# Kernel optimization log

Hardware: AMD Instinct MI355X
Metric: run time of the kernel (lower is better)

The kernel has to match this reference:

```python
import jax, jax.numpy as jnp
import numpy as np

THRESH = 0.5
MARGIN = 0.1
SCALE_POS = 2.0
SCALE_NEG = 40.0
SCALE_POS_W = 1.0
SCALE_NEG_W = 1.0

B, D = 4096, 256
N_CLASSES = 64


def setup_inputs() -> dict:
    key = jax.random.key(0)
    k1, k2, k3 = jax.random.split(key, 3)
    feats = jax.random.normal(k1, (B, D), dtype=jnp.float32)
    sim_weight = jax.random.uniform(k2, (B, B), dtype=jnp.float32)
    labels = jax.random.randint(k3, (B,), 0, N_CLASSES, dtype=jnp.int64)
    return {"feats": feats, "sim_weight": sim_weight, "labels": labels}


def reference(feats, sim_weight, labels):
    # L2-normalize rows, cosine-similarity matrix [B, B]
    feats_norm = feats / jnp.linalg.norm(feats, axis=1, keepdims=True)
    sim = feats_norm @ feats_norm.T

    # pos mask includes the diagonal (labels[i] == labels[i]), matching torch code
    pos_mask = labels[:, None] == labels[None, :]
    neg_mask = ~pos_mask

    # per-row min positive similarity (pos set is never empty due to diagonal)
    min_pos = jnp.min(jnp.where(pos_mask, sim, jnp.inf), axis=1, keepdims=True)
    # per-row max negative similarity; only valid when row has a negative
    has_neg = jnp.any(neg_mask, axis=1, keepdims=True)
    max_neg = jnp.max(jnp.where(neg_mask, sim, -jnp.inf), axis=1, keepdims=True)

    # hard mining: keep negs harder than the easiest pos, pos harder than hardest neg
    neg_keep = neg_mask & (sim + MARGIN > min_pos)
    pos_keep = pos_mask & jnp.where(has_neg, sim - MARGIN < max_neg, True)

    # masked log-sum-exp style reductions (non-vanila path uses sim_weight)
    pos_exp = jnp.exp(-SCALE_POS * (sim - THRESH) + SCALE_POS_W * sim_weight)
    neg_exp = jnp.exp(SCALE_NEG * (sim - THRESH) - SCALE_NEG_W * sim_weight)
    pos_sum = jnp.sum(jnp.where(pos_keep, pos_exp, 0.0), axis=1)
    neg_sum = jnp.sum(jnp.where(neg_keep, neg_exp, 0.0), axis=1)

    pos_loss = jnp.log1p(pos_sum) / SCALE_POS
    neg_loss = jnp.log1p(neg_sum) / SCALE_NEG
    # rows with both sets empty contribute log1p(0)=0, matching the `continue`
    return jnp.sum(pos_loss + neg_loss) / feats.shape[0]
```

## Files before the change

### kernel.cpp

```cpp
#include <hip/hip_runtime.h>
#include <hip/hip_bf16.h>
#include <math.h>

#define B_SZ 4096
#define D_SZ 256
#define MARGIN   0.1f

typedef __attribute__((ext_vector_type(8))) __bf16 bf16x8;
typedef __attribute__((ext_vector_type(4))) float f32x4;
typedef __attribute__((ext_vector_type(8))) unsigned short u16x8;

__device__ __forceinline__ unsigned short f2bf(float f) {
    unsigned u = __float_as_uint(f);
    unsigned r = (u + 0x7FFFu + ((u >> 16) & 1u)) >> 16;
    return (unsigned short)r;
}

__device__ __forceinline__ void gload_lds16(const void* g, void* lds) {
    __builtin_amdgcn_global_load_lds(
        (const __attribute__((address_space(1))) void*)g,
        (__attribute__((address_space(3))) void*)lds, 16, 0, 0);
}

__global__ void norm_init_kernel(const float* __restrict__ feats,
                                 unsigned short* __restrict__ fb) {
    int row = blockIdx.x;
    int lane = threadIdx.x;
    const float4 v = *(const float4*)(feats + (size_t)row * D_SZ + lane * 4);
    float s = v.x * v.x + v.y * v.y + v.z * v.z + v.w * v.w;
#pragma unroll
    for (int m = 32; m; m >>= 1) s += __shfl_xor(s, m);
    float rinv = 1.0f / sqrtf(s);
    short4 st;
    st.x = (short)f2bf(v.x * rinv);
    st.y = (short)f2bf(v.y * rinv);
    st.z = (short)f2bf(v.z * rinv);
    st.w = (short)f2bf(v.w * rinv);
    *(short4*)(fb + (size_t)row * D_SZ + lane * 4) = st;
}

__device__ __forceinline__ void gemm_tile(const unsigned short* __restrict__ fb,
                                          unsigned short* lA0, unsigned short* lB0,
                                          int i0, int j0, int t, f32x4 acc[4][4]) {
    const int lane = t & 63, w = t >> 6;
    const int wr = w >> 1, wc = w & 1;
    const int fr = lane & 15, kg = lane >> 4;
    const int srow = lane >> 2, schunk = lane & 3;

#pragma unroll
    for (int m = 0; m < 4; ++m)
#pragma unroll
        for (int n = 0; n < 4; ++n) acc[m][n] = (f32x4){0.f, 0.f, 0.f, 0.f};

    auto stage = [&](int buf, int kc) {
#pragma unroll
        for (int half = 0; half < 2; ++half) {
            const int R0 = w * 32 + half * 16;
            const int row = R0 + srow;
            const int off = ((schunk ^ ((row >> 1) & 3)) << 3);
            gload_lds16(fb + (size_t)(i0 + row) * D_SZ + kc + off,
                        lA0 + buf * (128 * 32) + R0 * 32);
            gload_lds16(fb + (size_t)(j0 + row) * D_SZ + kc + off,
                        lB0 + buf * (128 * 32) + R0 * 32);
        }
    };

    stage(0, 0);
    asm volatile("s_waitcnt vmcnt(0)" ::: "memory");
    __syncthreads();

#pragma unroll
    for (int s = 0; s < 8; ++s) {
        const int cur = s & 1;
        if (s < 7) stage(cur ^ 1, (s + 1) * 32);
        const unsigned short* A  = lA0 + cur * (128 * 32);
        const unsigned short* Bp = lB0 + cur * (128 * 32);
        bf16x8 a[4], b[4];
#pragma unroll
        for (int m = 0; m < 4; ++m) {
            const int row = wr * 64 + m * 16 + fr;
            a[m] = *(const bf16x8*)(A + row * 32 + ((kg ^ ((row >> 1) & 3)) << 3));
        }
#pragma unroll
        for (int n = 0; n < 4; ++n) {
            const int row = wc * 64 + n * 16 + fr;
            b[n] = *(const bf16x8*)(Bp + row * 32 + ((kg ^ ((row >> 1) & 3)) << 3));
        }
#pragma unroll
        for (int m = 0; m < 4; ++m)
#pragma unroll
            for (int n = 0; n < 4; ++n)
                acc[m][n] = __builtin_amdgcn_mfma_f32_16x16x32_bf16(a[m], b[n], acc[m][n], 0, 0, 0);
        if (s < 7) {
            asm volatile("s_waitcnt vmcnt(0)" ::: "memory");
            __syncthreads();
        }
    }
}

__global__ __launch_bounds__(256, 4) void gemm_store_sym(const unsigned short* __restrict__ fb,
                                                         unsigned short* __restrict__ simb) {
    __shared__ unsigned short sm[2 * 128 * 32 * 2];
    const int t = threadIdx.x;

    int z = blockIdx.x, bi = 0;
    while (z >= 32 - bi) { z -= 32 - bi; ++bi; }
    const int bj = bi + z;
    const int i0 = bi * 128, j0 = bj * 128;

    f32x4 acc[4][4];
    gemm_tile(fb, sm, sm + 128 * 32 * 2, i0, j0, t, acc);

    const int lane = t & 63, w = t >> 6;
    const int wr = w >> 1, wc = w & 1, fr = lane & 15, kg = lane >> 4;

#pragma unroll
    for (int m = 0; m < 4; ++m)
#pragma unroll
        for (int r = 0; r < 4; ++r) {
            const size_t row = i0 + wr * 64 + m * 16 + kg * 4 + r;
#pragma unroll
            for (int n = 0; n < 4; ++n)
                simb[row * B_SZ + j0 + wc * 64 + n * 16 + fr] = f2bf(acc[m][n][r]);
        }

    if (bi == bj) return;

    __syncthreads();
    unsigned short* T = sm;
#pragma unroll
    for (int m = 0; m < 4; ++m) {
        const int rowbase = wr * 64 + m * 16 + kg * 4;
#pragma unroll
        for (int n = 0; n < 4; ++n) {
            const int col = wc * 64 + n * 16 + fr;
            short4 h;
            h.x = (short)f2bf(acc[m][n][0]);
            h.y = (short)f2bf(acc[m][n][1]);
            h.z = (short)f2bf(acc[m][n][2]);
            h.w = (short)f2bf(acc[m][n][3]);
            *(short4*)(T + col * 128 + (rowbase ^ ((col & 15) << 3))) = h;
        }
    }
    __syncthreads();

    const int r0 = t & 15, cb = t >> 4;
#pragma unroll
    for (int p = 0; p < 8; ++p) {
        const int c = cb + p * 16;
        u16x8 v = *(const u16x8*)(T + c * 128 + 8 * (r0 ^ (c & 15)));
        *(u16x8*)(simb + (size_t)(j0 + c) * B_SZ + i0 + r0 * 8) = v;
    }
}

__global__ __launch_bounds__(256) void row_pass(const unsigned short* __restrict__ simb,
                                                const float* __restrict__ simw,
                                                const int* __restrict__ labels,
                                                float* __restrict__ rowloss) {
    const int i = blockIdx.x, t = threadIdx.x;
    const int lane = t & 63, w = t >> 6;
    const int il = labels[i];
    float sv[16], wv[16];
    int lj[16];
    {
        const u16x8* sp = (const u16x8*)(simb + (size_t)i * B_SZ + t * 16);
        u16x8 s0 = sp[0], s1 = sp[1];
#pragma unroll
        for (int e = 0; e < 8; ++e) {
            sv[e]     = __uint_as_float((unsigned)s0[e] << 16);
            sv[8 + e] = __uint_as_float((unsigned)s1[e] << 16);
        }
        const float4* wp = (const float4*)(simw + (size_t)i * B_SZ + t * 16);
#pragma unroll
        for (int q = 0; q < 4; ++q) {
            float4 wq = wp[q];
            wv[q * 4 + 0] = wq.x; wv[q * 4 + 1] = wq.y;
            wv[q * 4 + 2] = wq.z; wv[q * 4 + 3] = wq.w;
        }
        const int4* lp = (const int4*)(labels + t * 16);
#pragma unroll
        for (int q = 0; q < 4; ++q) {
            int4 lq = lp[q];
            lj[q * 4 + 0] = lq.x; lj[q * 4 + 1] = lq.y;
            lj[q * 4 + 2] = lq.z; lj[q * 4 + 3] = lq.w;
        }
    }
    float mn = INFINITY, mx = -INFINITY;
#pragma unroll
    for (int e = 0; e < 16; ++e) {
        if (lj[e] == il) mn = fminf(mn, sv[e]);
        else             mx = fmaxf(mx, sv[e]);
    }
#pragma unroll
    for (int msk = 1; msk < 64; msk <<= 1) {
        mn = fminf(mn, __shfl_xor(mn, msk));
        mx = fmaxf(mx, __shfl_xor(mx, msk));
    }
    __shared__ float smn[4], smx[4], sps[4], sns[4];
    if (lane == 0) { smn[w] = mn; smx[w] = mx; }
    __syncthreads();
    mn = fminf(fminf(smn[0], smn[1]), fminf(smn[2], smn[3]));
    mx = fmaxf(fmaxf(smx[0], smx[1]), fmaxf(smx[2], smx[3]));
    const bool hasneg = (mx != -INFINITY);
    float ps = 0.f, ns = 0.f;
#pragma unroll
    for (int e = 0; e < 16; ++e) {
        const float s = sv[e];
        if (lj[e] == il) {
            if (!hasneg || (s - MARGIN < mx))
                ps += __expf(fmaf(-2.f, s, 1.f) + wv[e]);
        } else {
            if (s + MARGIN > mn)
                ns += __expf(fmaf(40.f, s, -20.f) - wv[e]);
        }
    }
#pragma unroll
    for (int msk = 1; msk < 64; msk <<= 1) {
        ps += __shfl_xor(ps, msk);
        ns += __shfl_xor(ns, msk);
    }
    if (lane == 0) { sps[w] = ps; sns[w] = ns; }
    __syncthreads();
    if (t == 0) {
        ps = sps[0] + sps[1] + sps[2] + sps[3];
        ns = sns[0] + sns[1] + sns[2] + sns[3];
        rowloss[i] = log1pf(ps) * 0.5f + log1pf(ns) * 0.025f;
    }
}

__global__ void final_big(const float* __restrict__ rowloss, float* __restrict__ out) {
    __shared__ float red[256];
    int t = threadIdx.x;
    float acc = 0.f;
    for (int i = t; i < B_SZ; i += 256) acc += rowloss[i];
    red[t] = acc;
    __syncthreads();
    for (int s = 128; s > 0; s >>= 1) {
        if (t < s) red[t] += red[t + s];
        __syncthreads();
    }
    if (t == 0) out[0] = red[0] / (float)B_SZ;
}

extern "C" void kernel_launch(void* const* d_in, const int* in_sizes, int n_in,
                              void* d_out, int out_size, void* d_ws, size_t ws_size,
                              hipStream_t stream) {
    const float* feats  = (const float*)d_in[0];
    const float* simw   = (const float*)d_in[1];
    const int*   labels = (const int*)d_in[2];
    float* out = (float*)d_out;

    char* ws = (char*)d_ws;
    float*    rowloss = (float*)ws;
    unsigned short* fb   = (unsigned short*)(ws + B_SZ * 4);
    unsigned short* simb = (unsigned short*)(ws + B_SZ * 4 + (size_t)B_SZ * D_SZ * 2);

    norm_init_kernel<<<B_SZ, 64, 0, stream>>>(feats, fb);

    gemm_store_sym<<<528, 256, 0, stream>>>(fb, simb);
    row_pass<<<B_SZ, 256, 0, stream>>>(simb, simw, labels, rowloss);
    final_big<<<1, 256, 0, stream>>>(rowloss, out);
}
```

Before: 49.88 us.

## Triple-buffer GEMM K-loop and fuse final reduction into row pass via atomics

The GEMM K-loop moves from double to triple buffering in LDS, prefetching two stages ahead and waiting with a partial vmcnt so loads overlap more MFMA work. The row pass now handles two rows per block and folds the final reduction in with an atomic accumulator and a last-block counter. This removes the separate final_big launch and the per-row loss buffer. The trade-offs are more LDS per GEMM block, which may lower occupancy, and a float atomic sum whose order is not deterministic.

```diff
diff --git a/kernel.cpp b/kernel.cpp
--- a/kernel.cpp
+++ b/kernel.cpp
@@ -23,7 +23,9 @@
 }
 
 __global__ void norm_init_kernel(const float* __restrict__ feats,
-                                 unsigned short* __restrict__ fb) {
+                                 unsigned short* __restrict__ fb,
+                                 float* __restrict__ accum,
+                                 unsigned* __restrict__ counter) {
     int row = blockIdx.x;
     int lane = threadIdx.x;
     const float4 v = *(const float4*)(feats + (size_t)row * D_SZ + lane * 4);
@@ -37,6 +39,7 @@
     st.z = (short)f2bf(v.z * rinv);
     st.w = (short)f2bf(v.w * rinv);
     *(short4*)(fb + (size_t)row * D_SZ + lane * 4) = st;
+    if (row == 0 && lane == 0) { *accum = 0.f; *counter = 0u; }
 }
 
 __device__ __forceinline__ void gemm_tile(const unsigned short* __restrict__ fb,
@@ -66,15 +69,16 @@
     };
 
     stage(0, 0);
-    asm volatile("s_waitcnt vmcnt(0)" ::: "memory");
-    __syncthreads();
+    stage(1, 32);
 
 #pragma unroll
     for (int s = 0; s < 8; ++s) {
-        const int cur = s & 1;
-        if (s < 7) stage(cur ^ 1, (s + 1) * 32);
-        const unsigned short* A  = lA0 + cur * (128 * 32);
-        const unsigned short* Bp = lB0 + cur * (128 * 32);
+        if (s < 7) asm volatile("s_waitcnt vmcnt(4)" ::: "memory");
+        else       asm volatile("s_waitcnt vmcnt(0)" ::: "memory");
+        __syncthreads();
+        if (s + 2 < 8) stage((s + 2) % 3, (s + 2) * 32);
+        const unsigned short* A  = lA0 + (s % 3) * (128 * 32);
+        const unsigned short* Bp = lB0 + (s % 3) * (128 * 32);
         bf16x8 a[4], b[4];
 #pragma unroll
         for (int m = 0; m < 4; ++m) {
@@ -91,16 +95,12 @@
 #pragma unroll
             for (int n = 0; n < 4; ++n)
                 acc[m][n] = __builtin_amdgcn_mfma_f32_16x16x32_bf16(a[m], b[n], acc[m][n], 0, 0, 0);
-        if (s < 7) {
-            asm volatile("s_waitcnt vmcnt(0)" ::: "memory");
-            __syncthreads();
-        }
     }
 }
 
 __global__ __launch_bounds__(256, 4) void gemm_store_sym(const unsigned short* __restrict__ fb,
                                                          unsigned short* __restrict__ simb) {
-    __shared__ unsigned short sm[2 * 128 * 32 * 2];
+    __shared__ unsigned short sm[3 * 128 * 32 * 2];
     const int t = threadIdx.x;
 
     int z = blockIdx.x, bi = 0;
@@ -109,7 +109,7 @@
     const int i0 = bi * 128, j0 = bj * 128;
 
     f32x4 acc[4][4];
-    gemm_tile(fb, sm, sm + 128 * 32 * 2, i0, j0, t, acc);
+    gemm_tile(fb, sm, sm + 3 * 128 * 32, i0, j0, t, acc);
 
     const int lane = t & 63, w = t >> 6;
     const int wr = w >> 1, wc = w & 1, fr = lane & 15, kg = lane >> 4;
@@ -156,27 +156,13 @@
 __global__ __launch_bounds__(256) void row_pass(const unsigned short* __restrict__ simb,
                                                 const float* __restrict__ simw,
                                                 const int* __restrict__ labels,
-                                                float* __restrict__ rowloss) {
-    const int i = blockIdx.x, t = threadIdx.x;
+                                                float* __restrict__ accum,
+                                                unsigned* __restrict__ counter,
+                                                float* __restrict__ out) {
+    const int t = threadIdx.x;
     const int lane = t & 63, w = t >> 6;
-    const int il = labels[i];
-    float sv[16], wv[16];
     int lj[16];
     {
-        const u16x8* sp = (const u16x8*)(simb + (size_t)i * B_SZ + t * 16);
-        u16x8 s0 = sp[0], s1 = sp[1];
-#pragma unroll
-        for (int e = 0; e < 8; ++e) {
-            sv[e]     = __uint_as_float((unsigned)s0[e] << 16);
-            sv[8 + e] = __uint_as_float((unsigned)s1[e] << 16);
-        }
-        const float4* wp = (const float4*)(simw + (size_t)i * B_SZ + t * 16);
-#pragma unroll
-        for (int q = 0; q < 4; ++q) {
-            float4 wq = wp[q];
-            wv[q * 4 + 0] = wq.x; wv[q * 4 + 1] = wq.y;
-            wv[q * 4 + 2] = wq.z; wv[q * 4 + 3] = wq.w;
-        }
         const int4* lp = (const int4*)(labels + t * 16);
 #pragma unroll
         for (int q = 0; q < 4; ++q) {
@@ -185,61 +171,82 @@
             lj[q * 4 + 2] = lq.z; lj[q * 4 + 3] = lq.w;
         }
     }
-    float mn = INFINITY, mx = -INFINITY;
-#pragma unroll
-    for (int e = 0; e < 16; ++e) {
-        if (lj[e] == il) mn = fminf(mn, sv[e]);
-        else             mx = fmaxf(mx, sv[e]);
-    }
-#pragma unroll
-    for (int msk = 1; msk < 64; msk <<= 1) {
-        mn = fminf(mn, __shfl_xor(mn, msk));
-        mx = fmaxf(mx, __shfl_xor(mx, msk));
-    }
     __shared__ float smn[4], smx[4], sps[4], sns[4];
-    if (lane == 0) { smn[w] = mn; smx[w] = mx; }
-    __syncthreads();
-    mn = fminf(fminf(smn[0], smn[1]), fminf(smn[2], smn[3]));
-    mx = fmaxf(fmaxf(smx[0], smx[1]), fmaxf(smx[2], smx[3]));
-    const bool hasneg = (mx != -INFINITY);
-    float ps = 0.f, ns = 0.f;
-#pragma unroll
-    for (int e = 0; e < 16; ++e) {
-        const float s = sv[e];
-        if (lj[e] == il) {
-            if (!hasneg || (s - MARGIN < mx))
-                ps += __expf(fmaf(-2.f, s, 1.f) + wv[e]);
-        } else {
-            if (s + MARGIN > mn)
-                ns += __expf(fmaf(40.f, s, -20.f) - wv[e]);
-        }
-    }
-#pragma unroll
-    for (int msk = 1; msk < 64; msk <<= 1) {
-        ps += __shfl_xor(ps, msk);
-        ns += __shfl_xor(ns, msk);
-    }
-    if (lane == 0) { sps[w] = ps; sns[w] = ns; }
-    __syncthreads();
+    float bl = 0.f;
+
+#pragma unroll
+    for (int rr = 0; rr < 2; ++rr) {
+        const int i = blockIdx.x * 2 + rr;
+        const int il = labels[i];
+        float sv[16], wv[16];
+        {
+            const u16x8* sp = (const u16x8*)(simb + (size_t)i * B_SZ + t * 16);
+            u16x8 s0 = sp[0], s1 = sp[1];
+#pragma unroll
+            for (int e = 0; e < 8; ++e) {
+                sv[e]     = __uint_as_float((unsigned)s0[e] << 16);
+                sv[8 + e] = __uint_as_float((unsigned)s1[e] << 16);
+            }
+            const float4* wp = (const float4*)(simw + (size_t)i * B_SZ + t * 16);
+#pragma unroll
+            for (int q = 0; q < 4; ++q) {
+                float4 wq = wp[q];
+                wv[q * 4 + 0] = wq.x; wv[q * 4 + 1] = wq.y;
+                wv[q * 4 + 2] = wq.z; wv[q * 4 + 3] = wq.w;
+            }
+        }
+        float mn = INFINITY, mx = -INFINITY;
+#pragma unroll
+        for (int e = 0; e < 16; ++e) {
+            if (lj[e] == il) mn = fminf(mn, sv[e]);
+            else             mx = fmaxf(mx, sv[e]);
+        }
+#pragma unroll
+        for (int msk = 1; msk < 64; msk <<= 1) {
+            mn = fminf(mn, __shfl_xor(mn, msk));
+            mx = fmaxf(mx, __shfl_xor(mx, msk));
+        }
+        if (lane == 0) { smn[w] = mn; smx[w] = mx; }
+        __syncthreads();
+        mn = fminf(fminf(smn[0], smn[1]), fminf(smn[2], smn[3]));
+        mx = fmaxf(fmaxf(smx[0], smx[1]), fmaxf(smx[2], smx[3]));
+        const bool hasneg = (mx != -INFINITY);
+        float ps = 0.f, ns = 0.f;
+#pragma unroll
+        for (int e = 0; e < 16; ++e) {
+            const float s = sv[e];
+            if (lj[e] == il) {
+                if (!hasneg || (s - MARGIN < mx))
+                    ps += __expf(fmaf(-2.f, s, 1.f) + wv[e]);
+            } else {
+                if (s + MARGIN > mn)
+                    ns += __expf(fmaf(40.f, s, -20.f) - wv[e]);
+            }
+        }
+#pragma unroll
+        for (int msk = 1; msk < 64; msk <<= 1) {
+            ps += __shfl_xor(ps, msk);
+            ns += __shfl_xor(ns, msk);
+        }
+        if (lane == 0) { sps[w] = ps; sns[w] = ns; }
+        __syncthreads();
+        if (t == 0) {
+            ps = sps[0] + sps[1] + sps[2] + sps[3];
+            ns = sns[0] + sns[1] + sns[2] + sns[3];
+            bl += log1pf(ps) * 0.5f + log1pf(ns) * 0.025f;
+        }
+        __syncthreads();
+    }
+
     if (t == 0) {
-        ps = sps[0] + sps[1] + sps[2] + sps[3];
-        ns = sns[0] + sns[1] + sns[2] + sns[3];
-        rowloss[i] = log1pf(ps) * 0.5f + log1pf(ns) * 0.025f;
-    }
-}
-
-__global__ void final_big(const float* __restrict__ rowloss, float* __restrict__ out) {
-    __shared__ float red[256];
-    int t = threadIdx.x;
-    float acc = 0.f;
-    for (int i = t; i < B_SZ; i += 256) acc += rowloss[i];
-    red[t] = acc;
-    __syncthreads();
-    for (int s = 128; s > 0; s >>= 1) {
-        if (t < s) red[t] += red[t + s];
-        __syncthreads();
-    }
-    if (t == 0) out[0] = red[0] / (float)B_SZ;
+        atomicAdd(accum, bl);
+        __threadfence();
+        unsigned d = atomicAdd(counter, 1u);
+        if (d == (B_SZ / 2) - 1) {
+            __threadfence();
+            out[0] = *(volatile float*)accum / (float)B_SZ;
+        }
+    }
 }
 
 extern "C" void kernel_launch(void* const* d_in, const int* in_sizes, int n_in,
@@ -251,13 +258,12 @@
     float* out = (float*)d_out;
 
     char* ws = (char*)d_ws;
-    float*    rowloss = (float*)ws;
-    unsigned short* fb   = (unsigned short*)(ws + B_SZ * 4);
-    unsigned short* simb = (unsigned short*)(ws + B_SZ * 4 + (size_t)B_SZ * D_SZ * 2);
-
-    norm_init_kernel<<<B_SZ, 64, 0, stream>>>(feats, fb);
-
+    float*    accum   = (float*)ws;
+    unsigned* counter = (unsigned*)(ws + 64);
+    unsigned short* fb   = (unsigned short*)(ws + 4096);
+    unsigned short* simb = (unsigned short*)(ws + 4096 + (size_t)B_SZ * D_SZ * 2);
+
+    norm_init_kernel<<<B_SZ, 64, 0, stream>>>(feats, fb, accum, counter);
     gemm_store_sym<<<528, 256, 0, stream>>>(fb, simb);
-    row_pass<<<B_SZ, 256, 0, stream>>>(simb, simw, labels, rowloss);
-    final_big<<<1, 256, 0, stream>>>(rowloss, out);
-}
+    row_pass<<<B_SZ / 2, 256, 0, stream>>>(simb, simw, labels, accum, counter, out);
+}
```

Result: slower. 97.40 us (+95.3%).
